# Kernel optimization log

Hardware: AMD Instinct MI355X
Metric: run time of the kernel (lower is better)

The kernel has to match this reference:

```python
import jax, jax.numpy as jnp
import numpy as np

D_MODEL = 1024
N_HEADS = 16
D_K = D_MODEL // N_HEADS
B, S = 2, 2048


def setup_inputs() -> dict:
    key = jax.random.key(0)
    ks = jax.random.split(key, 12)
    sc = 1.0 / np.sqrt(D_MODEL)
    inp = {
        "Q": jax.random.normal(ks[0], (B, S, D_MODEL), jnp.float32),
        "K": jax.random.normal(ks[1], (B, S, D_MODEL), jnp.float32),
        "V": jax.random.normal(ks[2], (B, S, D_MODEL), jnp.float32),
        # causal mask: 0 where disallowed (masked_fill(mask==0, -inf))
        "mask": jnp.broadcast_to(jnp.tril(jnp.ones((S, S), jnp.int32))[None, None], (B, 1, S, S)),
        "Wq": jax.random.normal(ks[3], (D_MODEL, D_MODEL), jnp.float32) * sc,
        "bq": jnp.zeros((D_MODEL,), jnp.float32),
        "Wk": jax.random.normal(ks[4], (D_MODEL, D_MODEL), jnp.float32) * sc,
        "bk": jnp.zeros((D_MODEL,), jnp.float32),
        "Wv": jax.random.normal(ks[5], (D_MODEL, D_MODEL), jnp.float32) * sc,
        "bv": jnp.zeros((D_MODEL,), jnp.float32),
        "Wo": jax.random.normal(ks[6], (D_MODEL, D_MODEL), jnp.float32) * sc,
        "bo": jnp.zeros((D_MODEL,), jnp.float32),
    }
    return inp


def reference(Q, K, V, mask, Wq, bq, Wk, bk, Wv, bv, Wo, bo):
    b = Q.shape[0]
    # projections, split heads: [b, h, s, d_k]
    def proj(x, W, bias):
        y = x @ W.T + bias
        return y.reshape(b, -1, N_HEADS, D_K).transpose(0, 2, 1, 3)
    q = proj(Q, Wq, bq)
    k = proj(K, Wk, bk)
    v = proj(V, Wv, bv)
    scores = jnp.einsum('bhsd,bhtd->bhst', q, k) / jnp.sqrt(jnp.float32(D_K))
    scores = jnp.where(mask == 0, jnp.finfo(scores.dtype).min, scores)
    attn = jax.nn.softmax(scores, axis=-1)  # [b, h, s, s]
    out = jnp.einsum('bhst,bhtd->bhsd', attn, v)
    out = out.transpose(0, 2, 1, 3).reshape(b, -1, D_MODEL)
    out = out @ Wo.T + bo  # dropout is identity in eval mode
    return out, attn
```

## Files before the change

kernel.cpp:

```cpp
#include <hip/hip_runtime.h>
#include <math.h>

#define D_MODEL 1024
#define NH 16
#define DK 64
#define BB 2
#define SS 2048
#define BH (BB * NH)
#define M_TOT (BB * SS)
#define NQT (SS / 64)

typedef __bf16 bf16x8 __attribute__((ext_vector_type(8)));
typedef float f32x4 __attribute__((ext_vector_type(4)));

static __device__ __forceinline__ unsigned short f2bf(float x) {
  unsigned int u = __float_as_uint(x);
  u = (u + 0x7fffu + ((u >> 16) & 1u)) >> 16;
  return (unsigned short)u;
}

__global__ __launch_bounds__(256) void cvt_bf16_82592221102086(
    const float* __restrict__ src, unsigned short* __restrict__ dst, int n8) {
  int i = blockIdx.x * blockDim.x + threadIdx.x;
  if (i >= n8) return;
  const float4* s = reinterpret_cast<const float4*>(src) + 2 * (size_t)i;
  float4 a = s[0], b = s[1];
  union { unsigned short us[8]; uint4 u4; } pk;
  pk.us[0] = f2bf(a.x); pk.us[1] = f2bf(a.y);
  pk.us[2] = f2bf(a.z); pk.us[3] = f2bf(a.w);
  pk.us[4] = f2bf(b.x); pk.us[5] = f2bf(b.y);
  pk.us[6] = f2bf(b.z); pk.us[7] = f2bf(b.w);
  *(reinterpret_cast<uint4*>(dst) + i) = pk.u4;
}

template <int MODE>
__global__ __launch_bounds__(256) void proj_mfma_82592221102086(
    const unsigned short* __restrict__ X, const unsigned short* __restrict__ W,
    const float* __restrict__ bias, void* __restrict__ Yv) {
  __shared__ __align__(16) unsigned short As[128][72];
  __shared__ __align__(16) unsigned short Bs[64][72];
  const int tid = threadIdx.x;
  const int wave = tid >> 6, lane = tid & 63;
  const int lrow = lane & 15, lkc = lane >> 4;
  const int m0 = blockIdx.y * 128, n0 = blockIdx.x * 64;

  f32x4 acc[2][4] = {};

  for (int kt = 0; kt < D_MODEL; kt += 64) {
    __syncthreads();
#pragma unroll
    for (int i = 0; i < 4; ++i) {
      int c = tid + 256 * i, r = c >> 3, c8 = (c & 7) * 8;
      *reinterpret_cast<uint4*>(&As[r][c8]) = *reinterpret_cast<const uint4*>(
          &X[(size_t)(m0 + r) * D_MODEL + kt + c8]);
    }
#pragma unroll
    for (int i = 0; i < 2; ++i) {
      int c = tid + 256 * i, r = c >> 3, c8 = (c & 7) * 8;
      *reinterpret_cast<uint4*>(&Bs[r][c8]) = *reinterpret_cast<const uint4*>(
          &W[(size_t)(n0 + r) * D_MODEL + kt + c8]);
    }
    __syncthreads();
#pragma unroll
    for (int kk = 0; kk < 64; kk += 32) {
      bf16x8 a0 = *reinterpret_cast<const bf16x8*>(
          &As[wave * 32 + lrow][kk + lkc * 8]);
      bf16x8 a1 = *reinterpret_cast<const bf16x8*>(
          &As[wave * 32 + 16 + lrow][kk + lkc * 8]);
#pragma unroll
      for (int nj = 0; nj < 4; ++nj) {
        bf16x8 b = *reinterpret_cast<const bf16x8*>(
            &Bs[nj * 16 + lrow][kk + lkc * 8]);
        acc[0][nj] = __builtin_amdgcn_mfma_f32_16x16x32_bf16(a0, b, acc[0][nj], 0, 0, 0);
        acc[1][nj] = __builtin_amdgcn_mfma_f32_16x16x32_bf16(a1, b, acc[1][nj], 0, 0, 0);
      }
    }
  }

  const int h = n0 >> 6;
#pragma unroll
  for (int mi = 0; mi < 2; ++mi) {
#pragma unroll
    for (int nj = 0; nj < 4; ++nj) {
      const int d = nj * 16 + lrow;
      const float bv = bias[n0 + d];
#pragma unroll
      for (int j = 0; j < 4; ++j) {
        const int m = m0 + wave * 32 + mi * 16 + lkc * 4 + j;
        const float val = acc[mi][nj][j] + bv;
        if (MODE == 0) {
          const int b = m >> 11, s = m & 2047;
          reinterpret_cast<unsigned short*>(Yv)
              [((size_t)(b * NH + h) * SS + s) * DK + d] = f2bf(val);
        } else {
          reinterpret_cast<float*>(Yv)[(size_t)m * D_MODEL + n0 + d] = val;
        }
      }
    }
  }
}

__global__ __launch_bounds__(256) void attn_mfma_82592221102086(
    const unsigned short* __restrict__ qb, const unsigned short* __restrict__ kb,
    const unsigned short* __restrict__ vb, float* __restrict__ attn,
    unsigned short* __restrict__ ctx) {
  __shared__ __align__(16) unsigned short Ks[64][72];
  __shared__ __align__(16) unsigned short Vt[64][72];
  __shared__ __align__(16) unsigned short Ps[64][72];
  const int bi = blockIdx.x;
  const int xcd = bi & 7, slot = bi >> 3;
  const int bh = xcd * 4 + (slot >> 5);
  const int qt = slot & 31;
  const int qs = qt * 64;
  const int tid = threadIdx.x;
  const int wave = tid >> 6, lane = tid & 63;
  const int lrow = lane & 15, lkc = lane >> 4;

  const unsigned short* qrow =
      qb + ((size_t)bh * SS + qs + wave * 16 + lrow) * DK;
  bf16x8 qf[2];
  qf[0] = *reinterpret_cast<const bf16x8*>(qrow + lkc * 8);
  qf[1] = *reinterpret_cast<const bf16x8*>(qrow + 32 + lkc * 8);

  float lsum[4] = {};

  for (int kt = 0; kt <= qt; ++kt) {
    const int ks = kt * 64;
    __syncthreads();
#pragma unroll
    for (int i = 0; i < 2; ++i) {
      int c = tid + 256 * i, r = c >> 3, c8 = (c & 7) * 8;
      *reinterpret_cast<uint4*>(&Ks[r][c8]) = *reinterpret_cast<const uint4*>(
          &kb[((size_t)bh * SS + ks + r) * DK + c8]);
    }
    __syncthreads();

    f32x4 sacc[4] = {};
#pragma unroll
    for (int kk = 0; kk < 64; kk += 32) {
      const int idx = kk >> 5;
#pragma unroll
      for (int tj = 0; tj < 4; ++tj) {
        bf16x8 kf = *reinterpret_cast<const bf16x8*>(
            &Ks[tj * 16 + lrow][kk + lkc * 8]);
        sacc[tj] = __builtin_amdgcn_mfma_f32_16x16x32_bf16(qf[idx], kf, sacc[tj], 0, 0, 0);
      }
    }
    const bool diag = (kt == qt);
#pragma unroll
    for (int tj = 0; tj < 4; ++tj) {
#pragma unroll
      for (int j = 0; j < 4; ++j) {
        const int grow = qs + wave * 16 + lkc * 4 + j;
        const int gcol = ks + tj * 16 + lrow;
        if (!diag || gcol <= grow)
          lsum[j] += __expf(fminf(sacc[tj][j] * 0.125f, 80.f));
      }
    }
  }

  float inv[4];
#pragma unroll
  for (int j = 0; j < 4; ++j) {
    float l = lsum[j];
#pragma unroll
    for (int m = 1; m < 16; m <<= 1) l += __shfl_xor(l, m, 64);
    inv[j] = 1.0f / l;
  }

  f32x4 oacc[4] = {};

  for (int kt = 0; kt <= qt; ++kt) {
    const int ks = kt * 64;
    __syncthreads();
#pragma unroll
    for (int i = 0; i < 2; ++i) {
      int c = tid + 256 * i, r = c >> 3, c8 = (c & 7) * 8;
      *reinterpret_cast<uint4*>(&Ks[r][c8]) = *reinterpret_cast<const uint4*>(
          &kb[((size_t)bh * SS + ks + r) * DK + c8]);
    }
#pragma unroll
    for (int i = 0; i < 2; ++i) {
      int c = tid + 256 * i, t = c >> 3, d0 = (c & 7) * 8;
      uint4 raw = *reinterpret_cast<const uint4*>(
          &vb[((size_t)bh * SS + ks + t) * DK + d0]);
      const unsigned short* pv = reinterpret_cast<const unsigned short*>(&raw);
      const int tsw = t ^ d0;
#pragma unroll
      for (int jj = 0; jj < 8; ++jj) Vt[d0 + jj][tsw] = pv[jj];
    }
    __syncthreads();

    f32x4 sacc[4] = {};
#pragma unroll
    for (int kk = 0; kk < 64; kk += 32) {
      const int idx = kk >> 5;
#pragma unroll
      for (int tj = 0; tj < 4; ++tj) {
        bf16x8 kf = *reinterpret_cast<const bf16x8*>(
            &Ks[tj * 16 + lrow][kk + lkc * 8]);
        sacc[tj] = __builtin_amdgcn_mfma_f32_16x16x32_bf16(qf[idx], kf, sacc[tj], 0, 0, 0);
      }
    }

    const bool diag = (kt == qt);
#pragma unroll
    for (int tj = 0; tj < 4; ++tj) {
#pragma unroll
      for (int j = 0; j < 4; ++j) {
        const int prow = lkc * 4 + j;
        const int grow = qs + wave * 16 + prow;
        const int gcol = ks + tj * 16 + lrow;
        float pv = 0.f;
        if (!diag || gcol <= grow)
          pv = __expf(fminf(sacc[tj][j] * 0.125f, 80.f)) * inv[j];
        __builtin_nontemporal_store(
            pv, &attn[((size_t)bh * SS + grow) * SS + gcol]);
        Ps[wave * 16 + prow][tj * 16 + lrow] = f2bf(pv);
      }
    }
#pragma unroll
    for (int kk2 = 0; kk2 < 64; kk2 += 32) {
      bf16x8 pf = *reinterpret_cast<const bf16x8*>(
          &Ps[wave * 16 + lrow][kk2 + lkc * 8]);
#pragma unroll
      for (int dj = 0; dj < 4; ++dj) {
        const int d = dj * 16 + lrow;
        const int tch = ((kk2 >> 3) + lkc) ^ (d >> 3);
        bf16x8 vf = *reinterpret_cast<const bf16x8*>(&Vt[d][tch << 3]);
        oacc[dj] = __builtin_amdgcn_mfma_f32_16x16x32_bf16(pf, vf, oacc[dj], 0, 0, 0);
      }
    }
  }

  const int b = bh >> 4, h = bh & 15;
#pragma unroll
  for (int dj = 0; dj < 4; ++dj) {
    const int d = dj * 16 + lrow;
#pragma unroll
    for (int j = 0; j < 4; ++j) {
      const int row = qs + wave * 16 + lkc * 4 + j;
      ctx[((size_t)(b * SS + row)) * D_MODEL + h * DK + d] =
          f2bf(oacc[dj][j]);
    }
  }

  const f32x4 z4 = {0.f, 0.f, 0.f, 0.f};
  for (int kt = qt + 1; kt < NQT; ++kt) {
    const int ks = kt * 64;
#pragma unroll
    for (int u = 0; u < 4; ++u) {
      const int idx = tid + 256 * u;
      const int r = idx >> 4, c4 = idx & 15;
      __builtin_nontemporal_store(
          z4, reinterpret_cast<f32x4*>(
                  &attn[((size_t)bh * SS + qs + r) * SS + ks + c4 * 4]));
    }
  }
}

extern "C" void kernel_launch(void* const* d_in, const int* in_sizes, int n_in,
                              void* d_out, int out_size, void* d_ws,
                              size_t ws_size, hipStream_t stream) {
  const float* Q = (const float*)d_in[0];
  const float* K = (const float*)d_in[1];
  const float* V = (const float*)d_in[2];
  const float* Wq = (const float*)d_in[4];
  const float* bq = (const float*)d_in[5];
  const float* Wk = (const float*)d_in[6];
  const float* bk = (const float*)d_in[7];
  const float* Wv = (const float*)d_in[8];
  const float* bv = (const float*)d_in[9];
  const float* Wo = (const float*)d_in[10];
  const float* bo = (const float*)d_in[11];

  float* out = (float*)d_out;
  float* attn = out + (size_t)M_TOT * D_MODEL;

  const size_t nX = (size_t)M_TOT * D_MODEL;
  const size_t nW = (size_t)D_MODEL * D_MODEL;
  unsigned short* ws = (unsigned short*)d_ws;
  unsigned short* Qc = ws;
  unsigned short* Kc = Qc + nX;
  unsigned short* Vc = Kc + nX;
  unsigned short* Wqc = Vc + nX;
  unsigned short* Wkc = Wqc + nW;
  unsigned short* Wvc = Wkc + nW;
  unsigned short* Woc = Wvc + nW;
  unsigned short* qbv = Woc + nW;
  unsigned short* kbv = qbv + nX;
  unsigned short* vbv = kbv + nX;
  unsigned short* ctx = vbv + nX;

  cvt_bf16_82592221102086<<<(nX / 8 + 255) / 256, 256, 0, stream>>>(Q, Qc, nX / 8);
  cvt_bf16_82592221102086<<<(nX / 8 + 255) / 256, 256, 0, stream>>>(K, Kc, nX / 8);
  cvt_bf16_82592221102086<<<(nX / 8 + 255) / 256, 256, 0, stream>>>(V, Vc, nX / 8);
  cvt_bf16_82592221102086<<<(nW / 8 + 255) / 256, 256, 0, stream>>>(Wq, Wqc, nW / 8);
  cvt_bf16_82592221102086<<<(nW / 8 + 255) / 256, 256, 0, stream>>>(Wk, Wkc, nW / 8);
  cvt_bf16_82592221102086<<<(nW / 8 + 255) / 256, 256, 0, stream>>>(Wv, Wvc, nW / 8);
  cvt_bf16_82592221102086<<<(nW / 8 + 255) / 256, 256, 0, stream>>>(Wo, Woc, nW / 8);

  const dim3 gGemm(D_MODEL / 64, M_TOT / 128);
  proj_mfma_82592221102086<0><<<gGemm, 256, 0, stream>>>(Qc, Wqc, bq, qbv);
  proj_mfma_82592221102086<0><<<gGemm, 256, 0, stream>>>(Kc, Wkc, bk, kbv);
  proj_mfma_82592221102086<0><<<gGemm, 256, 0, stream>>>(Vc, Wvc, bv, vbv);

  attn_mfma_82592221102086<<<dim3(NQT * BH), 256, 0, stream>>>(
      qbv, kbv, vbv, attn, ctx);

  proj_mfma_82592221102086<1><<<gGemm, 256, 0, stream>>>(ctx, Woc, bo, out);
}
```

Before: 888.5 us.

## Merge conversion and QKV launches, enlarge attention query block, stage attn stores

```diff
diff --git a/kernel.cpp b/kernel.cpp
--- a/kernel.cpp
+++ b/kernel.cpp
@@ -8,7 +8,8 @@
 #define SS 2048
 #define BH (BB * NH)
 #define M_TOT (BB * SS)
-#define NQT (SS / 64)
+#define QBLK 128
+#define NSTRIP (SS / QBLK)
 
 typedef __bf16 bf16x8 __attribute__((ext_vector_type(8)));
 typedef float f32x4 __attribute__((ext_vector_type(4)));
@@ -19,30 +20,47 @@
   return (unsigned short)u;
 }
 
-__global__ __launch_bounds__(256) void cvt_bf16_82592221102086(
-    const float* __restrict__ src, unsigned short* __restrict__ dst, int n8) {
-  int i = blockIdx.x * blockDim.x + threadIdx.x;
-  if (i >= n8) return;
-  const float4* s = reinterpret_cast<const float4*>(src) + 2 * (size_t)i;
-  float4 a = s[0], b = s[1];
+__global__ __launch_bounds__(256) void cvt_all_82592221102086(
+    const float* __restrict__ Q, const float* __restrict__ K,
+    const float* __restrict__ V, const float* __restrict__ Wq,
+    const float* __restrict__ Wk, const float* __restrict__ Wv,
+    const float* __restrict__ Wo, unsigned short* __restrict__ Qc,
+    unsigned short* __restrict__ Kc, unsigned short* __restrict__ Vc,
+    unsigned short* __restrict__ Wqc, unsigned short* __restrict__ Wkc,
+    unsigned short* __restrict__ Wvc, unsigned short* __restrict__ Woc) {
+  const int id = blockIdx.x;
+  const float* s;
+  unsigned short* d;
+  int c0;
+  if (id < 2048) { s = Q; d = Qc; c0 = id * 256; }
+  else if (id < 4096) { s = K; d = Kc; c0 = (id - 2048) * 256; }
+  else if (id < 6144) { s = V; d = Vc; c0 = (id - 4096) * 256; }
+  else {
+    const int w = (id - 6144) >> 9, off = (id - 6144) & 511;
+    s = (w == 0) ? Wq : (w == 1) ? Wk : (w == 2) ? Wv : Wo;
+    d = (w == 0) ? Wqc : (w == 1) ? Wkc : (w == 2) ? Wvc : Woc;
+    c0 = off * 256;
+  }
+  const size_t i = (size_t)c0 + threadIdx.x;
+  const float4* sp = reinterpret_cast<const float4*>(s) + 2 * i;
+  float4 a = sp[0], b = sp[1];
   union { unsigned short us[8]; uint4 u4; } pk;
   pk.us[0] = f2bf(a.x); pk.us[1] = f2bf(a.y);
   pk.us[2] = f2bf(a.z); pk.us[3] = f2bf(a.w);
   pk.us[4] = f2bf(b.x); pk.us[5] = f2bf(b.y);
   pk.us[6] = f2bf(b.z); pk.us[7] = f2bf(b.w);
-  *(reinterpret_cast<uint4*>(dst) + i) = pk.u4;
+  *(reinterpret_cast<uint4*>(d) + i) = pk.u4;
 }
 
 template <int MODE>
-__global__ __launch_bounds__(256) void proj_mfma_82592221102086(
+static __device__ __forceinline__ void proj_body(
     const unsigned short* __restrict__ X, const unsigned short* __restrict__ W,
-    const float* __restrict__ bias, void* __restrict__ Yv) {
+    const float* __restrict__ bias, void* __restrict__ Yv, int m0, int n0) {
   __shared__ __align__(16) unsigned short As[128][72];
   __shared__ __align__(16) unsigned short Bs[64][72];
   const int tid = threadIdx.x;
   const int wave = tid >> 6, lane = tid & 63;
   const int lrow = lane & 15, lkc = lane >> 4;
-  const int m0 = blockIdx.y * 128, n0 = blockIdx.x * 64;
 
   f32x4 acc[2][4] = {};
 
@@ -100,36 +118,61 @@
   }
 }
 
-__global__ __launch_bounds__(256) void attn_mfma_82592221102086(
+__global__ __launch_bounds__(256) void proj_qkv_82592221102086(
+    const unsigned short* __restrict__ Qc, const unsigned short* __restrict__ Kc,
+    const unsigned short* __restrict__ Vc, const unsigned short* __restrict__ Wqc,
+    const unsigned short* __restrict__ Wkc, const unsigned short* __restrict__ Wvc,
+    const float* __restrict__ bq, const float* __restrict__ bk,
+    const float* __restrict__ bv, unsigned short* __restrict__ qbv,
+    unsigned short* __restrict__ kbv, unsigned short* __restrict__ vbv) {
+  const unsigned short *X, *W;
+  const float* bias;
+  unsigned short* Y;
+  if (blockIdx.z == 0) { X = Qc; W = Wqc; bias = bq; Y = qbv; }
+  else if (blockIdx.z == 1) { X = Kc; W = Wkc; bias = bk; Y = kbv; }
+  else { X = Vc; W = Wvc; bias = bv; Y = vbv; }
+  proj_body<0>(X, W, bias, Y, blockIdx.y * 128, blockIdx.x * 64);
+}
+
+__global__ __launch_bounds__(256) void proj_out_82592221102086(
+    const unsigned short* __restrict__ X, const unsigned short* __restrict__ W,
+    const float* __restrict__ bias, float* __restrict__ Y) {
+  proj_body<1>(X, W, bias, Y, blockIdx.y * 128, blockIdx.x * 64);
+}
+
+__global__ __launch_bounds__(512, 4) void attn_mfma_82592221102086(
     const unsigned short* __restrict__ qb, const unsigned short* __restrict__ kb,
     const unsigned short* __restrict__ vb, float* __restrict__ attn,
     unsigned short* __restrict__ ctx) {
   __shared__ __align__(16) unsigned short Ks[64][72];
   __shared__ __align__(16) unsigned short Vt[64][72];
-  __shared__ __align__(16) unsigned short Ps[64][72];
+  __shared__ __align__(16) unsigned short Ps[QBLK][76];
+  __shared__ __align__(16) float Pf[QBLK][76];
+
   const int bi = blockIdx.x;
   const int xcd = bi & 7, slot = bi >> 3;
-  const int bh = xcd * 4 + (slot >> 5);
-  const int qt = slot & 31;
-  const int qs = qt * 64;
+  const int bhl = (slot >> 4) & 3;
+  const int bh = xcd * 4 + bhl;
+  const int u = slot & 15;
+  const int qt = (bhl & 2) ? (15 - u) : u;
+  const int qs = qt * QBLK;
+  const int ntile = 2 * qt + 2;
   const int tid = threadIdx.x;
   const int wave = tid >> 6, lane = tid & 63;
   const int lrow = lane & 15, lkc = lane >> 4;
 
   const unsigned short* qrow =
       qb + ((size_t)bh * SS + qs + wave * 16 + lrow) * DK;
-  bf16x8 qf[2];
-  qf[0] = *reinterpret_cast<const bf16x8*>(qrow + lkc * 8);
-  qf[1] = *reinterpret_cast<const bf16x8*>(qrow + 32 + lkc * 8);
+  const bf16x8 qf0 = *reinterpret_cast<const bf16x8*>(qrow + lkc * 8);
+  const bf16x8 qf1 = *reinterpret_cast<const bf16x8*>(qrow + 32 + lkc * 8);
 
   float lsum[4] = {};
 
-  for (int kt = 0; kt <= qt; ++kt) {
+  for (int kt = 0; kt < ntile; ++kt) {
     const int ks = kt * 64;
     __syncthreads();
-#pragma unroll
-    for (int i = 0; i < 2; ++i) {
-      int c = tid + 256 * i, r = c >> 3, c8 = (c & 7) * 8;
+    {
+      const int r = tid >> 3, c8 = (tid & 7) * 8;
       *reinterpret_cast<uint4*>(&Ks[r][c8]) = *reinterpret_cast<const uint4*>(
           &kb[((size_t)bh * SS + ks + r) * DK + c8]);
     }
@@ -138,15 +181,15 @@
     f32x4 sacc[4] = {};
 #pragma unroll
     for (int kk = 0; kk < 64; kk += 32) {
-      const int idx = kk >> 5;
+      const bf16x8 qf = (kk == 0) ? qf0 : qf1;
 #pragma unroll
       for (int tj = 0; tj < 4; ++tj) {
         bf16x8 kf = *reinterpret_cast<const bf16x8*>(
             &Ks[tj * 16 + lrow][kk + lkc * 8]);
-        sacc[tj] = __builtin_amdgcn_mfma_f32_16x16x32_bf16(qf[idx], kf, sacc[tj], 0, 0, 0);
-      }
-    }
-    const bool diag = (kt == qt);
+        sacc[tj] = __builtin_amdgcn_mfma_f32_16x16x32_bf16(qf, kf, sacc[tj], 0, 0, 0);
+      }
+    }
+    const bool diag = (kt >= ntile - 2);
 #pragma unroll
     for (int tj = 0; tj < 4; ++tj) {
 #pragma unroll
@@ -170,18 +213,16 @@
 
   f32x4 oacc[4] = {};
 
-  for (int kt = 0; kt <= qt; ++kt) {
+  for (int kt = 0; kt < ntile; ++kt) {
     const int ks = kt * 64;
     __syncthreads();
-#pragma unroll
-    for (int i = 0; i < 2; ++i) {
-      int c = tid + 256 * i, r = c >> 3, c8 = (c & 7) * 8;
+    {
+      const int r = tid >> 3, c8 = (tid & 7) * 8;
       *reinterpret_cast<uint4*>(&Ks[r][c8]) = *reinterpret_cast<const uint4*>(
           &kb[((size_t)bh * SS + ks + r) * DK + c8]);
     }
-#pragma unroll
-    for (int i = 0; i < 2; ++i) {
-      int c = tid + 256 * i, t = c >> 3, d0 = (c & 7) * 8;
+    {
+      const int t = tid >> 3, d0 = (tid & 7) * 8;
       uint4 raw = *reinterpret_cast<const uint4*>(
           &vb[((size_t)bh * SS + ks + t) * DK + d0]);
       const unsigned short* pv = reinterpret_cast<const unsigned short*>(&raw);
@@ -194,31 +235,41 @@
     f32x4 sacc[4] = {};
 #pragma unroll
     for (int kk = 0; kk < 64; kk += 32) {
-      const int idx = kk >> 5;
+      const bf16x8 qf = (kk == 0) ? qf0 : qf1;
 #pragma unroll
       for (int tj = 0; tj < 4; ++tj) {
         bf16x8 kf = *reinterpret_cast<const bf16x8*>(
             &Ks[tj * 16 + lrow][kk + lkc * 8]);
-        sacc[tj] = __builtin_amdgcn_mfma_f32_16x16x32_bf16(qf[idx], kf, sacc[tj], 0, 0, 0);
-      }
-    }
-
-    const bool diag = (kt == qt);
+        sacc[tj] = __builtin_amdgcn_mfma_f32_16x16x32_bf16(qf, kf, sacc[tj], 0, 0, 0);
+      }
+    }
+
+    const bool diag = (kt >= ntile - 2);
 #pragma unroll
     for (int tj = 0; tj < 4; ++tj) {
 #pragma unroll
       for (int j = 0; j < 4; ++j) {
-        const int prow = lkc * 4 + j;
-        const int grow = qs + wave * 16 + prow;
+        const int prow = wave * 16 + lkc * 4 + j;
+        const int grow = qs + prow;
         const int gcol = ks + tj * 16 + lrow;
         float pv = 0.f;
         if (!diag || gcol <= grow)
           pv = __expf(fminf(sacc[tj][j] * 0.125f, 80.f)) * inv[j];
-        __builtin_nontemporal_store(
-            pv, &attn[((size_t)bh * SS + grow) * SS + gcol]);
-        Ps[wave * 16 + prow][tj * 16 + lrow] = f2bf(pv);
-      }
-    }
+        Pf[prow][tj * 16 + lrow] = pv;
+        Ps[prow][tj * 16 + lrow] = f2bf(pv);
+      }
+    }
+    __syncthreads();
+
+#pragma unroll
+    for (int it = 0; it < 4; ++it) {
+      const int r = it * 32 + (tid >> 4), c0 = (tid & 15) * 4;
+      const f32x4 v = *reinterpret_cast<const f32x4*>(&Pf[r][c0]);
+      __builtin_nontemporal_store(
+          v, reinterpret_cast<f32x4*>(
+                 &attn[((size_t)bh * SS + qs + r) * SS + ks + c0]));
+    }
+
 #pragma unroll
     for (int kk2 = 0; kk2 < 64; kk2 += 32) {
       bf16x8 pf = *reinterpret_cast<const bf16x8*>(
@@ -240,21 +291,19 @@
 #pragma unroll
     for (int j = 0; j < 4; ++j) {
       const int row = qs + wave * 16 + lkc * 4 + j;
-      ctx[((size_t)(b * SS + row)) * D_MODEL + h * DK + d] =
-          f2bf(oacc[dj][j]);
+      ctx[((size_t)(b * SS + row)) * D_MODEL + h * DK + d] = f2bf(oacc[dj][j]);
     }
   }
 
   const f32x4 z4 = {0.f, 0.f, 0.f, 0.f};
-  for (int kt = qt + 1; kt < NQT; ++kt) {
+  for (int kt = ntile; kt < 32; ++kt) {
     const int ks = kt * 64;
 #pragma unroll
-    for (int u = 0; u < 4; ++u) {
-      const int idx = tid + 256 * u;
-      const int r = idx >> 4, c4 = idx & 15;
+    for (int it = 0; it < 4; ++it) {
+      const int r = it * 32 + (tid >> 4), c0 = (tid & 15) * 4;
       __builtin_nontemporal_store(
           z4, reinterpret_cast<f32x4*>(
-                  &attn[((size_t)bh * SS + qs + r) * SS + ks + c4 * 4]));
+                  &attn[((size_t)bh * SS + qs + r) * SS + ks + c0]));
     }
   }
 }
@@ -292,21 +341,16 @@
   unsigned short* vbv = kbv + nX;
   unsigned short* ctx = vbv + nX;
 
-  cvt_bf16_82592221102086<<<(nX / 8 + 255) / 256, 256, 0, stream>>>(Q, Qc, nX / 8);
-  cvt_bf16_82592221102086<<<(nX / 8 + 255) / 256, 256, 0, stream>>>(K, Kc, nX / 8);
-  cvt_bf16_82592221102086<<<(nX / 8 + 255) / 256, 256, 0, stream>>>(V, Vc, nX / 8);
-  cvt_bf16_82592221102086<<<(nW / 8 + 255) / 256, 256, 0, stream>>>(Wq, Wqc, nW / 8);
-  cvt_bf16_82592221102086<<<(nW / 8 + 255) / 256, 256, 0, stream>>>(Wk, Wkc, nW / 8);
-  cvt_bf16_82592221102086<<<(nW / 8 + 255) / 256, 256, 0, stream>>>(Wv, Wvc, nW / 8);
-  cvt_bf16_82592221102086<<<(nW / 8 + 255) / 256, 256, 0, stream>>>(Wo, Woc, nW / 8);
-
-  const dim3 gGemm(D_MODEL / 64, M_TOT / 128);
-  proj_mfma_82592221102086<0><<<gGemm, 256, 0, stream>>>(Qc, Wqc, bq, qbv);
-  proj_mfma_82592221102086<0><<<gGemm, 256, 0, stream>>>(Kc, Wkc, bk, kbv);
-  proj_mfma_82592221102086<0><<<gGemm, 256, 0, stream>>>(Vc, Wvc, bv, vbv);
-
-  attn_mfma_82592221102086<<<dim3(NQT * BH), 256, 0, stream>>>(
+  cvt_all_82592221102086<<<8192, 256, 0, stream>>>(
+      Q, K, V, Wq, Wk, Wv, Wo, Qc, Kc, Vc, Wqc, Wkc, Wvc, Woc);
+
+  proj_qkv_82592221102086<<<dim3(D_MODEL / 64, M_TOT / 128, 3), 256, 0,
+                            stream>>>(Qc, Kc, Vc, Wqc, Wkc, Wvc, bq, bk, bv,
+                                      qbv, kbv, vbv);
+
+  attn_mfma_82592221102086<<<dim3(BH * NSTRIP), 512, 0, stream>>>(
       qbv, kbv, vbv, attn, ctx);
 
-  proj_mfma_82592221102086<1><<<gGemm, 256, 0, stream>>>(ctx, Woc, bo, out);
-}
+  proj_out_82592221102086<<<dim3(D_MODEL / 64, M_TOT / 128), 256, 0, stream>>>(
+      ctx, Woc, bo, out);
+}
```

Result: faster. 789.5 us (-11.1%).
